# Kernel optimization log

Measured on AMD Instinct MI355X. Metric: run time of the kernel, lower is better.

## Reference

```python
import jax, jax.numpy as jnp
import numpy as np

DT = 1e-4  # integration step, matches Model(dt=0.0001)
T = 4_000_000


def setup_inputs() -> dict:
    key = jax.random.key(0)
    ks = jax.random.split(key, 8)
    inputs = jax.random.normal(ks[0], (1, T, 3), dtype=jnp.float32)
    # time column made increasing (as in a real signal record)
    t = jnp.arange(T, dtype=jnp.float32) * DT
    inputs = inputs.at[0, :, 0].set(t)
    # small-scale 2x2 system matrices; A shifted toward -0.5*I so the
    # 4M-step linear recurrence is stable (no overflow over long horizons)
    A = -0.5 * jnp.eye(2, dtype=jnp.float32) + 0.05 * jax.random.normal(ks[1], (2, 2), jnp.float32)
    B = 0.1 * jax.random.normal(ks[2], (2, 2), jnp.float32)
    D = 0.1 * jax.random.normal(ks[3], (2, 2), jnp.float32)
    E = 0.1 * jax.random.normal(ks[4], (2, 2), jnp.float32)
    cov_in = 0.1 * jax.random.normal(ks[5], (2, 2), jnp.float32)
    training_params = jax.random.normal(ks[6], (1, 2), jnp.float32)
    initial_states = jnp.zeros((1, 5), dtype=jnp.float32)
    return {"inputs": inputs, "A": A, "B": B, "D": D, "E": E,
            "cov_in": cov_in, "training_params": training_params,
            "initial_states": initial_states}


def reference(inputs, A, B, D, E, cov_in, training_params, initial_states):
    # Faithful to GRCell.call: cov = cov_in every step (new_cov is discarded),
    # so XiCov / XiCovC / transition matrix are time-invariant constants.
    dt = jnp.float32(DT)
    sqrt2 = jnp.sqrt(jnp.float32(2.0))
    x_signal = jnp.array([1.0, 0.0], dtype=inputs.dtype)
    XiCov = (E - cov_in @ B) / sqrt2                      # (2,2)
    XiCovC = XiCov @ (-sqrt2 * B.T)                       # (2,2)
    Trans = jnp.eye(2, dtype=inputs.dtype) + (A - XiCovC) * dt  # I + (A-XiCovC)dt
    Cout = -sqrt2 * B.T * dt                              # output map, (2,2)
    p0 = training_params[0, 0]
    p1 = training_params[0, 1]
    seq = inputs[0]                                       # [T, 3] = (time, dy1, dy2)

    def step(x, inp):
        t = inp[0]
        dy = inp[1:]
        out = Cout @ x                                    # emitted BEFORE update
        x_new = Trans @ x + XiCov @ dy + (p0 * jnp.cos(p1 * t) * dt) * x_signal
        return x_new, out

    x0 = initial_states[0, :2]
    _, outs = jax.lax.scan(step, x0, seq)                 # outs: [T, 2]
    return outs[None]                                     # [1, T, 2]
```

## Files before the change

### kernel.cpp

```cpp
#include <hip/hip_runtime.h>
#include <math.h>


constexpr int   TN    = 4000000;
constexpr float FDT   = 1e-4f;
constexpr int   L     = 16;
constexpr int   K     = TN / L;
constexpr int   BT    = 256;
constexpr int   NT    = (K + BT - 1) / BT;
constexpr int   ROWF4 = 9;
constexpr int   F4IN  = TN * 3 / 4;
constexpr int   F4OUT = TN * 2 / 4;

struct Consts {
  float T00, T01, T10, T11;
  float X00, X01, X10, X11;
  float C00, C01, C10, C11;
  float p0, p1;
};

__device__ inline Consts make_consts(const float* __restrict__ A,
                                     const float* __restrict__ B,
                                     const float* __restrict__ E,
                                     const float* __restrict__ cov,
                                     const float* __restrict__ tp) {
  const float s2 = 1.41421356237309515f;
  Consts c;
  float Xi[2][2];
  for (int i = 0; i < 2; ++i)
    for (int j = 0; j < 2; ++j)
      Xi[i][j] = (E[i*2+j] - (cov[i*2+0]*B[0*2+j] + cov[i*2+1]*B[1*2+j])) / s2;
  float XiC[2][2];
  for (int i = 0; i < 2; ++i)
    for (int j = 0; j < 2; ++j)
      XiC[i][j] = Xi[i][0]*(-s2*B[j*2+0]) + Xi[i][1]*(-s2*B[j*2+1]);
  c.T00 = 1.0f + (A[0] - XiC[0][0]) * FDT;
  c.T01 =        (A[1] - XiC[0][1]) * FDT;
  c.T10 =        (A[2] - XiC[1][0]) * FDT;
  c.T11 = 1.0f + (A[3] - XiC[1][1]) * FDT;
  c.X00 = Xi[0][0]; c.X01 = Xi[0][1]; c.X10 = Xi[1][0]; c.X11 = Xi[1][1];
  c.C00 = -s2 * B[0] * FDT;
  c.C01 = -s2 * B[2] * FDT;
  c.C10 = -s2 * B[1] * FDT;
  c.C11 = -s2 * B[3] * FDT;
  c.p0 = tp[0]; c.p1 = tp[1];
  return c;
}

__device__ inline void step(float& x0, float& x1, float t, float a, float b,
                            const Consts& c) {
  float u0 = fmaf(c.X00, a, fmaf(c.X01, b, c.p0 * __cosf(c.p1 * t) * FDT));
  float u1 = fmaf(c.X10, a, c.X11 * b);
  float n0 = fmaf(c.T00, x0, fmaf(c.T01, x1, u0));
  float n1 = fmaf(c.T10, x0, fmaf(c.T11, x1, u1));
  x0 = n0; x1 = n1;
}

__device__ inline void fsq(float* M) {
  float a = M[0]*M[0] + M[1]*M[2];
  float b = M[0]*M[1] + M[1]*M[3];
  float d = M[2]*M[0] + M[3]*M[2];
  float e = M[2]*M[1] + M[3]*M[3];
  M[0] = a; M[1] = b; M[2] = d; M[3] = e;
}

__device__ inline void mulleft(const float* P, float* M) {
  float a0 = P[0]*M[0] + P[1]*M[2];
  float a1 = P[0]*M[1] + P[1]*M[3];
  float a2 = P[2]*M[0] + P[3]*M[2];
  float a3 = P[2]*M[1] + P[3]*M[3];
  M[0]=a0; M[1]=a1; M[2]=a2; M[3]=a3;
}

__device__ inline void powmat8(const float* M, int e, float* R) {
  float C[4] = {M[0], M[1], M[2], M[3]};
  R[0] = 1.f; R[1] = 0.f; R[2] = 0.f; R[3] = 1.f;
  #pragma unroll
  for (int b = 0; b < 8; ++b) {
    if ((e >> b) & 1) mulleft(C, R);
    fsq(C);
  }
}

__global__ void __launch_bounds__(BT, 4)
k1(const float* __restrict__ seq, const float* __restrict__ A,
   const float* __restrict__ B, const float* __restrict__ E,
   const float* __restrict__ cov, const float* __restrict__ tp,
   float2* __restrict__ agg) {
  __shared__ float wg[4][2];
  const int tid  = threadIdx.x;
  const int lane = tid & 63;
  const int w    = tid >> 6;
  const int tile = blockIdx.x;
  Consts c = make_consts(A, B, E, cov, tp);

  const float4* s4 = (const float4*)seq;
  const size_t base = (size_t)tile * 3072 + 3 * tid;
  const float4 z4 = make_float4(0.f, 0.f, 0.f, 0.f);
  float4 v[12];
  #pragma unroll
  for (int it = 0; it < 4; ++it) {
    size_t g = base + (size_t)(it * 768);
    v[3*it+0] = (g     < (size_t)F4IN) ? s4[g]     : z4;
    v[3*it+1] = (g + 1 < (size_t)F4IN) ? s4[g + 1] : z4;
    v[3*it+2] = (g + 2 < (size_t)F4IN) ? s4[g + 2] : z4;
  }

  float S[4] = {c.T00, c.T01, c.T10, c.T11};
  fsq(S); fsq(S);
  float R[4];
  powmat8(S, 255 - tid, R);
  float S256[4] = {S[0], S[1], S[2], S[3]};
  #pragma unroll
  for (int i = 0; i < 8; ++i) fsq(S256);

  float acc0 = 0.f, acc1 = 0.f;
  #pragma unroll
  for (int it = 3; it >= 0; --it) {
    float x0 = 0.f, x1 = 0.f;
    const float4 a = v[3*it], b = v[3*it+1], d = v[3*it+2];
    const int st0 = tile * 4096 + 1024 * it + 4 * tid;
    step(x0, x1, (float)(st0    ) * FDT, a.y, a.z, c);
    step(x0, x1, (float)(st0 + 1) * FDT, b.x, b.y, c);
    step(x0, x1, (float)(st0 + 2) * FDT, b.w, d.x, c);
    step(x0, x1, (float)(st0 + 3) * FDT, d.z, d.w, c);
    if (it != 3) mulleft(S256, R);
    acc0 += R[0]*x0 + R[1]*x1;
    acc1 += R[2]*x0 + R[3]*x1;
  }

  #pragma unroll
  for (int m = 1; m < 64; m <<= 1) {
    acc0 += __shfl_xor(acc0, m);
    acc1 += __shfl_xor(acc1, m);
  }
  if (lane == 0) { wg[w][0] = acc0; wg[w][1] = acc1; }
  __syncthreads();
  if (tid == 0) {
    float a0 = wg[0][0] + wg[1][0] + wg[2][0] + wg[3][0];
    float a1 = wg[0][1] + wg[1][1] + wg[2][1] + wg[3][1];
    agg[tile] = make_float2(a0, a1);
  }
}

__device__ inline void stage_tile(const float4* __restrict__ seq4, int tile,
                                  float4* __restrict__ ls, int tid) {
  const size_t base4 = (size_t)tile * 3072;
  #pragma unroll
  for (int it = 0; it < 4; ++it) {
    const int u = it * BT + tid;
    const size_t g = base4 + (size_t)(it * 768 + 3 * tid);
    float4 v0 = make_float4(0.f,0.f,0.f,0.f);
    float4 v1 = v0, v2 = v0;
    if (g     < (size_t)F4IN) v0 = seq4[g];
    if (g + 1 < (size_t)F4IN) v1 = seq4[g + 1];
    if (g + 2 < (size_t)F4IN) v2 = seq4[g + 2];
    const int st  = u >> 2;
    const int kq  = u & 3;
    const int rot = (st >> 3) & 7;
    float4* row = ls + st * ROWF4;
    row[(2*kq     + rot) & 7] = make_float4(v0.y, v0.z, v1.x, v1.y);
    row[(2*kq + 1 + rot) & 7] = make_float4(v1.w, v2.x, v2.z, v2.w);
  }
}

__global__ void __launch_bounds__(BT, 4)
k3(const float* __restrict__ seq, const float* __restrict__ A,
   const float* __restrict__ B, const float* __restrict__ E,
   const float* __restrict__ cov, const float* __restrict__ tp,
   const float* __restrict__ ini, const float2* __restrict__ agg,
   float* __restrict__ out) {
  __shared__ float4 ls[BT * ROWF4];
  __shared__ float  wg[4][2];
  __shared__ float  sY[2];
  const int tid  = threadIdx.x;
  const int lane = tid & 63;
  const int w    = tid >> 6;
  const int tile = blockIdx.x;
  Consts c = make_consts(A, B, E, cov, tp);

  stage_tile((const float4*)seq, tile, ls, tid);

  {
    float Qb[4] = {c.T00, c.T01, c.T10, c.T11};
    #pragma unroll
    for (int i = 0; i < 12; ++i) fsq(Qb);
    float i0 = 0.f, i1 = 0.f;
    float inc[4][2];
    #pragma unroll
    for (int j = 0; j < 4; ++j) {
      int idx = 4 * tid + j;
      float e0 = 0.f, e1 = 0.f;
      if (idx == 0)      { e0 = ini[0]; e1 = ini[1]; }
      else if (idx < NT) { float2 a = agg[idx-1]; e0 = a.x; e1 = a.y; }
      float n0 = fmaf(Qb[0], i0, fmaf(Qb[1], i1, e0));
      float n1 = fmaf(Qb[2], i0, fmaf(Qb[3], i1, e1));
      i0 = n0; i1 = n1;
      inc[j][0] = i0; inc[j][1] = i1;
    }
    float Q4[4] = {Qb[0], Qb[1], Qb[2], Qb[3]};
    fsq(Q4); fsq(Q4);
    float C[4] = {Q4[0], Q4[1], Q4[2], Q4[3]};
    float v0 = i0, v1 = i1;
    #pragma unroll
    for (int s = 0; s < 6; ++s) {
      int st = 1 << s;
      float p0 = __shfl_up(v0, st);
      float p1 = __shfl_up(v1, st);
      if (lane >= st) {
        float n0 = fmaf(C[0], p0, fmaf(C[1], p1, v0));
        float n1 = fmaf(C[2], p0, fmaf(C[3], p1, v1));
        v0 = n0; v1 = n1;
      }
      fsq(C);
    }
    if (lane == 63) { wg[w][0] = v0; wg[w][1] = v1; }
    __syncthreads();
    float F0 = 0.f, F1 = 0.f;
    for (int ww = 0; ww < w; ++ww) {
      float n0 = fmaf(C[0], F0, fmaf(C[1], F1, wg[ww][0]));
      float n1 = fmaf(C[2], F0, fmaf(C[3], F1, wg[ww][1]));
      F0 = n0; F1 = n1;
    }
    float q0 = __shfl_up(v0, 1);
    float q1 = __shfl_up(v1, 1);
    if (lane == 0) { q0 = 0.f; q1 = 0.f; }
    float Mq[4];
    powmat8(Q4, lane, Mq);
    float Eth0 = fmaf(Mq[0], F0, fmaf(Mq[1], F1, q0));
    float Eth1 = fmaf(Mq[2], F0, fmaf(Mq[3], F1, q1));
    if (tid == (tile >> 2)) {
      int j = tile & 3;
      float Rj[4] = {Qb[0], Qb[1], Qb[2], Qb[3]};
      for (int m = 0; m < j; ++m) mulleft(Qb, Rj);
      sY[0] = fmaf(Rj[0], Eth0, fmaf(Rj[1], Eth1, inc[j][0]));
      sY[1] = fmaf(Rj[2], Eth0, fmaf(Rj[3], Eth1, inc[j][1]));
    }
    __syncthreads();
  }

  float Pb[4] = {c.T00, c.T01, c.T10, c.T11};
  #pragma unroll
  for (int i = 0; i < 4; ++i) fsq(Pb);
  float4* row = &ls[tid * ROWF4];
  const int rot = (tid >> 3) & 7;
  const int gstep = (tile * BT + tid) * L;
  float xe0, xe1;
  {
    float x0 = 0.f, x1 = 0.f;
    #pragma unroll
    for (int q = 0; q < 8; ++q) {
      float4 d = row[(q + rot) & 7];
      step(x0, x1, (float)(gstep + 2*q)     * FDT, d.x, d.y, c);
      step(x0, x1, (float)(gstep + 2*q + 1) * FDT, d.z, d.w, c);
    }
    float C[4] = {Pb[0], Pb[1], Pb[2], Pb[3]};
    float v0 = x0, v1 = x1;
    #pragma unroll
    for (int s = 0; s < 6; ++s) {
      int st = 1 << s;
      float p0 = __shfl_up(v0, st);
      float p1 = __shfl_up(v1, st);
      if (lane >= st) {
        float n0 = fmaf(C[0], p0, fmaf(C[1], p1, v0));
        float n1 = fmaf(C[2], p0, fmaf(C[3], p1, v1));
        v0 = n0; v1 = n1;
      }
      fsq(C);
    }
    if (lane == 63) { wg[w][0] = v0; wg[w][1] = v1; }
    __syncthreads();
    float E0 = 0.f, E1 = 0.f;
    for (int ww = 0; ww < w; ++ww) {
      float n0 = fmaf(C[0], E0, fmaf(C[1], E1, wg[ww][0]));
      float n1 = fmaf(C[2], E0, fmaf(C[3], E1, wg[ww][1]));
      E0 = n0; E1 = n1;
    }
    float pv0 = __shfl_up(v0, 1);
    float pv1 = __shfl_up(v1, 1);
    if (lane == 0) { pv0 = 0.f; pv1 = 0.f; }
    float Ml[4];
    powmat8(Pb, lane, Ml);
    xe0 = fmaf(Ml[0], E0, fmaf(Ml[1], E1, pv0));
    xe1 = fmaf(Ml[2], E0, fmaf(Ml[3], E1, pv1));
  }

  float Mt[4];
  powmat8(Pb, tid, Mt);
  float y0 = sY[0], y1 = sY[1];
  float x0 = fmaf(Mt[0], y0, fmaf(Mt[1], y1, xe0));
  float x1 = fmaf(Mt[2], y0, fmaf(Mt[3], y1, xe1));

  #pragma unroll
  for (int q = 0; q < 8; ++q) {
    float4 d = row[(q + rot) & 7];
    float4 o;
    o.x = fmaf(c.C00, x0, c.C01 * x1); o.y = fmaf(c.C10, x0, c.C11 * x1);
    step(x0, x1, (float)(gstep + 2*q) * FDT, d.x, d.y, c);
    o.z = fmaf(c.C00, x0, c.C01 * x1); o.w = fmaf(c.C10, x0, c.C11 * x1);
    step(x0, x1, (float)(gstep + 2*q + 1) * FDT, d.z, d.w, c);
    row[(q + rot) & 7] = o;
  }
  __syncthreads();

  float4* out4 = (float4*)out;
  const size_t obase = (size_t)tile * 2048;
  #pragma unroll
  for (int i = 0; i < 8; ++i) {
    int lf = i * BT + tid;
    size_t g = obase + (size_t)lf;
    if (g < (size_t)F4OUT) {
      int cc = lf >> 3, s = lf & 7;
      int rc = (cc >> 3) & 7;
      out4[g] = ls[cc * ROWF4 + ((s + rc) & 7)];
    }
  }
}

extern "C" void kernel_launch(void* const* d_in, const int* in_sizes, int n_in,
                              void* d_out, int out_size, void* d_ws, size_t ws_size,
                              hipStream_t stream) {
  const float* seq = (const float*)d_in[0];
  const float* A   = (const float*)d_in[1];
  const float* B   = (const float*)d_in[2];
  const float* E   = (const float*)d_in[4];
  const float* cov = (const float*)d_in[5];
  const float* tp  = (const float*)d_in[6];
  const float* ini = (const float*)d_in[7];
  float* out = (float*)d_out;

  float2* agg = (float2*)d_ws;

  k1<<<NT, BT, 0, stream>>>(seq, A, B, E, cov, tp, agg);
  k3<<<NT, BT, 0, stream>>>(seq, A, B, E, cov, tp, ini, agg, out);
}
```

Baseline: 124.0 us.

## Fuse the two scan passes into one cooperative kernel with a grid-wide sync

The two kernels are merged into one cooperative kernel. Each block stages its input tile in LDS once, computes its local scan and block aggregate, waits at a grid-wide barrier, then resolves the cross-block carry and writes its outputs from the same staged data. This drops the second full read of the input sequence and one kernel launch. In exchange it needs every block resident at once, since the barrier deadlocks otherwise, and it pays for a grid-sync. If the cooperative launch is rejected, it falls back to the old two-kernel path.

```diff
diff --git a/kernel.cpp b/kernel.cpp
--- a/kernel.cpp
+++ b/kernel.cpp
@@ -1,5 +1,8 @@
 #include <hip/hip_runtime.h>
+#include <hip/hip_cooperative_groups.h>
 #include <math.h>
+
+namespace cg = cooperative_groups;
 
 
 constexpr int   TN    = 4000000;
@@ -82,67 +85,6 @@
   }
 }
 
-__global__ void __launch_bounds__(BT, 4)
-k1(const float* __restrict__ seq, const float* __restrict__ A,
-   const float* __restrict__ B, const float* __restrict__ E,
-   const float* __restrict__ cov, const float* __restrict__ tp,
-   float2* __restrict__ agg) {
-  __shared__ float wg[4][2];
-  const int tid  = threadIdx.x;
-  const int lane = tid & 63;
-  const int w    = tid >> 6;
-  const int tile = blockIdx.x;
-  Consts c = make_consts(A, B, E, cov, tp);
-
-  const float4* s4 = (const float4*)seq;
-  const size_t base = (size_t)tile * 3072 + 3 * tid;
-  const float4 z4 = make_float4(0.f, 0.f, 0.f, 0.f);
-  float4 v[12];
-  #pragma unroll
-  for (int it = 0; it < 4; ++it) {
-    size_t g = base + (size_t)(it * 768);
-    v[3*it+0] = (g     < (size_t)F4IN) ? s4[g]     : z4;
-    v[3*it+1] = (g + 1 < (size_t)F4IN) ? s4[g + 1] : z4;
-    v[3*it+2] = (g + 2 < (size_t)F4IN) ? s4[g + 2] : z4;
-  }
-
-  float S[4] = {c.T00, c.T01, c.T10, c.T11};
-  fsq(S); fsq(S);
-  float R[4];
-  powmat8(S, 255 - tid, R);
-  float S256[4] = {S[0], S[1], S[2], S[3]};
-  #pragma unroll
-  for (int i = 0; i < 8; ++i) fsq(S256);
-
-  float acc0 = 0.f, acc1 = 0.f;
-  #pragma unroll
-  for (int it = 3; it >= 0; --it) {
-    float x0 = 0.f, x1 = 0.f;
-    const float4 a = v[3*it], b = v[3*it+1], d = v[3*it+2];
-    const int st0 = tile * 4096 + 1024 * it + 4 * tid;
-    step(x0, x1, (float)(st0    ) * FDT, a.y, a.z, c);
-    step(x0, x1, (float)(st0 + 1) * FDT, b.x, b.y, c);
-    step(x0, x1, (float)(st0 + 2) * FDT, b.w, d.x, c);
-    step(x0, x1, (float)(st0 + 3) * FDT, d.z, d.w, c);
-    if (it != 3) mulleft(S256, R);
-    acc0 += R[0]*x0 + R[1]*x1;
-    acc1 += R[2]*x0 + R[3]*x1;
-  }
-
-  #pragma unroll
-  for (int m = 1; m < 64; m <<= 1) {
-    acc0 += __shfl_xor(acc0, m);
-    acc1 += __shfl_xor(acc1, m);
-  }
-  if (lane == 0) { wg[w][0] = acc0; wg[w][1] = acc1; }
-  __syncthreads();
-  if (tid == 0) {
-    float a0 = wg[0][0] + wg[1][0] + wg[2][0] + wg[3][0];
-    float a1 = wg[0][1] + wg[1][1] + wg[2][1] + wg[3][1];
-    agg[tile] = make_float2(a0, a1);
-  }
-}
-
 __device__ inline void stage_tile(const float4* __restrict__ seq4, int tile,
                                   float4* __restrict__ ls, int tid) {
   const size_t base4 = (size_t)tile * 3072;
@@ -165,6 +107,229 @@
 }
 
 __global__ void __launch_bounds__(BT, 4)
+fused(const float* __restrict__ seq, const float* __restrict__ A,
+      const float* __restrict__ B, const float* __restrict__ E,
+      const float* __restrict__ cov, const float* __restrict__ tp,
+      const float* __restrict__ ini, float2* __restrict__ agg,
+      float* __restrict__ out) {
+  __shared__ float4 ls[BT * ROWF4];
+  __shared__ float  wg[4][2];
+  __shared__ float  sY[2];
+  const int tid  = threadIdx.x;
+  const int lane = tid & 63;
+  const int w    = tid >> 6;
+  const int tile = blockIdx.x;
+  Consts c = make_consts(A, B, E, cov, tp);
+
+  stage_tile((const float4*)seq, tile, ls, tid);
+  __syncthreads();
+
+  float Pb[4] = {c.T00, c.T01, c.T10, c.T11};
+  #pragma unroll
+  for (int i = 0; i < 4; ++i) fsq(Pb);
+  float4* row = &ls[tid * ROWF4];
+  const int rot = (tid >> 3) & 7;
+  const int gstep = (tile * BT + tid) * L;
+
+  float xe0, xe1;
+  {
+    float x0 = 0.f, x1 = 0.f;
+    #pragma unroll
+    for (int q = 0; q < 8; ++q) {
+      float4 d = row[(q + rot) & 7];
+      step(x0, x1, (float)(gstep + 2*q)     * FDT, d.x, d.y, c);
+      step(x0, x1, (float)(gstep + 2*q + 1) * FDT, d.z, d.w, c);
+    }
+    float C[4] = {Pb[0], Pb[1], Pb[2], Pb[3]};
+    float v0 = x0, v1 = x1;
+    #pragma unroll
+    for (int s = 0; s < 6; ++s) {
+      int st = 1 << s;
+      float p0 = __shfl_up(v0, st);
+      float p1 = __shfl_up(v1, st);
+      if (lane >= st) {
+        float n0 = fmaf(C[0], p0, fmaf(C[1], p1, v0));
+        float n1 = fmaf(C[2], p0, fmaf(C[3], p1, v1));
+        v0 = n0; v1 = n1;
+      }
+      fsq(C);
+    }
+    if (lane == 63) { wg[w][0] = v0; wg[w][1] = v1; }
+    __syncthreads();
+    float E0 = 0.f, E1 = 0.f;
+    for (int ww = 0; ww < w; ++ww) {
+      float n0 = fmaf(C[0], E0, fmaf(C[1], E1, wg[ww][0]));
+      float n1 = fmaf(C[2], E0, fmaf(C[3], E1, wg[ww][1]));
+      E0 = n0; E1 = n1;
+    }
+    float pv0 = __shfl_up(v0, 1);
+    float pv1 = __shfl_up(v1, 1);
+    if (lane == 0) { pv0 = 0.f; pv1 = 0.f; }
+    float Ml[4];
+    powmat8(Pb, lane, Ml);
+    xe0 = fmaf(Ml[0], E0, fmaf(Ml[1], E1, pv0));
+    xe1 = fmaf(Ml[2], E0, fmaf(Ml[3], E1, pv1));
+    if (tid == BT - 1) {
+      float a0 = fmaf(C[0], E0, fmaf(C[1], E1, v0));
+      float a1 = fmaf(C[2], E0, fmaf(C[3], E1, v1));
+      agg[tile] = make_float2(a0, a1);
+    }
+  }
+
+  cg::this_grid().sync();
+
+  {
+    float Qb[4] = {c.T00, c.T01, c.T10, c.T11};
+    #pragma unroll
+    for (int i = 0; i < 12; ++i) fsq(Qb);
+    float i0 = 0.f, i1 = 0.f;
+    float inc[4][2];
+    #pragma unroll
+    for (int j = 0; j < 4; ++j) {
+      int idx = 4 * tid + j;
+      float e0 = 0.f, e1 = 0.f;
+      if (idx == 0)      { e0 = ini[0]; e1 = ini[1]; }
+      else if (idx < NT) { float2 a = agg[idx-1]; e0 = a.x; e1 = a.y; }
+      float n0 = fmaf(Qb[0], i0, fmaf(Qb[1], i1, e0));
+      float n1 = fmaf(Qb[2], i0, fmaf(Qb[3], i1, e1));
+      i0 = n0; i1 = n1;
+      inc[j][0] = i0; inc[j][1] = i1;
+    }
+    float Q4[4] = {Qb[0], Qb[1], Qb[2], Qb[3]};
+    fsq(Q4); fsq(Q4);
+    float C[4] = {Q4[0], Q4[1], Q4[2], Q4[3]};
+    float v0 = i0, v1 = i1;
+    #pragma unroll
+    for (int s = 0; s < 6; ++s) {
+      int st = 1 << s;
+      float p0 = __shfl_up(v0, st);
+      float p1 = __shfl_up(v1, st);
+      if (lane >= st) {
+        float n0 = fmaf(C[0], p0, fmaf(C[1], p1, v0));
+        float n1 = fmaf(C[2], p0, fmaf(C[3], p1, v1));
+        v0 = n0; v1 = n1;
+      }
+      fsq(C);
+    }
+    if (lane == 63) { wg[w][0] = v0; wg[w][1] = v1; }
+    __syncthreads();
+    float F0 = 0.f, F1 = 0.f;
+    for (int ww = 0; ww < w; ++ww) {
+      float n0 = fmaf(C[0], F0, fmaf(C[1], F1, wg[ww][0]));
+      float n1 = fmaf(C[2], F0, fmaf(C[3], F1, wg[ww][1]));
+      F0 = n0; F1 = n1;
+    }
+    float q0 = __shfl_up(v0, 1);
+    float q1 = __shfl_up(v1, 1);
+    if (lane == 0) { q0 = 0.f; q1 = 0.f; }
+    float Mq[4];
+    powmat8(Q4, lane, Mq);
+    float Eth0 = fmaf(Mq[0], F0, fmaf(Mq[1], F1, q0));
+    float Eth1 = fmaf(Mq[2], F0, fmaf(Mq[3], F1, q1));
+    if (tid == (tile >> 2)) {
+      int j = tile & 3;
+      float Rj[4] = {Qb[0], Qb[1], Qb[2], Qb[3]};
+      for (int m = 0; m < j; ++m) mulleft(Qb, Rj);
+      sY[0] = fmaf(Rj[0], Eth0, fmaf(Rj[1], Eth1, inc[j][0]));
+      sY[1] = fmaf(Rj[2], Eth0, fmaf(Rj[3], Eth1, inc[j][1]));
+    }
+    __syncthreads();
+  }
+
+  float Mt[4];
+  powmat8(Pb, tid, Mt);
+  float y0 = sY[0], y1 = sY[1];
+  float x0 = fmaf(Mt[0], y0, fmaf(Mt[1], y1, xe0));
+  float x1 = fmaf(Mt[2], y0, fmaf(Mt[3], y1, xe1));
+
+  #pragma unroll
+  for (int q = 0; q < 8; ++q) {
+    float4 d = row[(q + rot) & 7];
+    float4 o;
+    o.x = fmaf(c.C00, x0, c.C01 * x1); o.y = fmaf(c.C10, x0, c.C11 * x1);
+    step(x0, x1, (float)(gstep + 2*q) * FDT, d.x, d.y, c);
+    o.z = fmaf(c.C00, x0, c.C01 * x1); o.w = fmaf(c.C10, x0, c.C11 * x1);
+    step(x0, x1, (float)(gstep + 2*q + 1) * FDT, d.z, d.w, c);
+    row[(q + rot) & 7] = o;
+  }
+  __syncthreads();
+
+  float4* out4 = (float4*)out;
+  const size_t obase = (size_t)tile * 2048;
+  #pragma unroll
+  for (int i = 0; i < 8; ++i) {
+    int lf = i * BT + tid;
+    size_t g = obase + (size_t)lf;
+    if (g < (size_t)F4OUT) {
+      int cc = lf >> 3, s = lf & 7;
+      int rc = (cc >> 3) & 7;
+      out4[g] = ls[cc * ROWF4 + ((s + rc) & 7)];
+    }
+  }
+}
+
+__global__ void __launch_bounds__(BT, 4)
+k1(const float* __restrict__ seq, const float* __restrict__ A,
+   const float* __restrict__ B, const float* __restrict__ E,
+   const float* __restrict__ cov, const float* __restrict__ tp,
+   float2* __restrict__ agg) {
+  __shared__ float wg[4][2];
+  const int tid  = threadIdx.x;
+  const int lane = tid & 63;
+  const int w    = tid >> 6;
+  const int tile = blockIdx.x;
+  Consts c = make_consts(A, B, E, cov, tp);
+
+  const float4* s4 = (const float4*)seq;
+  const size_t base = (size_t)tile * 3072 + 3 * tid;
+  const float4 z4 = make_float4(0.f, 0.f, 0.f, 0.f);
+  float4 v[12];
+  #pragma unroll
+  for (int it = 0; it < 4; ++it) {
+    size_t g = base + (size_t)(it * 768);
+    v[3*it+0] = (g     < (size_t)F4IN) ? s4[g]     : z4;
+    v[3*it+1] = (g + 1 < (size_t)F4IN) ? s4[g + 1] : z4;
+    v[3*it+2] = (g + 2 < (size_t)F4IN) ? s4[g + 2] : z4;
+  }
+
+  float S[4] = {c.T00, c.T01, c.T10, c.T11};
+  fsq(S); fsq(S);
+  float R[4];
+  powmat8(S, 255 - tid, R);
+  float S256[4] = {S[0], S[1], S[2], S[3]};
+  #pragma unroll
+  for (int i = 0; i < 8; ++i) fsq(S256);
+
+  float acc0 = 0.f, acc1 = 0.f;
+  #pragma unroll
+  for (int it = 3; it >= 0; --it) {
+    float x0 = 0.f, x1 = 0.f;
+    const float4 a = v[3*it], b = v[3*it+1], d = v[3*it+2];
+    const int st0 = tile * 4096 + 1024 * it + 4 * tid;
+    step(x0, x1, (float)(st0    ) * FDT, a.y, a.z, c);
+    step(x0, x1, (float)(st0 + 1) * FDT, b.x, b.y, c);
+    step(x0, x1, (float)(st0 + 2) * FDT, b.w, d.x, c);
+    step(x0, x1, (float)(st0 + 3) * FDT, d.z, d.w, c);
+    if (it != 3) mulleft(S256, R);
+    acc0 += R[0]*x0 + R[1]*x1;
+    acc1 += R[2]*x0 + R[3]*x1;
+  }
+
+  #pragma unroll
+  for (int m = 1; m < 64; m <<= 1) {
+    acc0 += __shfl_xor(acc0, m);
+    acc1 += __shfl_xor(acc1, m);
+  }
+  if (lane == 0) { wg[w][0] = acc0; wg[w][1] = acc1; }
+  __syncthreads();
+  if (tid == 0) {
+    float a0 = wg[0][0] + wg[1][0] + wg[2][0] + wg[3][0];
+    float a1 = wg[0][1] + wg[1][1] + wg[2][1] + wg[3][1];
+    agg[tile] = make_float2(a0, a1);
+  }
+}
+
+__global__ void __launch_bounds__(BT, 4)
 k3(const float* __restrict__ seq, const float* __restrict__ A,
    const float* __restrict__ B, const float* __restrict__ E,
    const float* __restrict__ cov, const float* __restrict__ tp,
@@ -331,6 +496,12 @@
 
   float2* agg = (float2*)d_ws;
 
-  k1<<<NT, BT, 0, stream>>>(seq, A, B, E, cov, tp, agg);
-  k3<<<NT, BT, 0, stream>>>(seq, A, B, E, cov, tp, ini, agg, out);
-}
+  void* args[] = {(void*)&seq, (void*)&A, (void*)&B, (void*)&E, (void*)&cov,
+                  (void*)&tp, (void*)&ini, (void*)&agg, (void*)&out};
+  hipError_t err = hipLaunchCooperativeKernel((void*)fused, dim3(NT), dim3(BT),
+                                              args, 0, stream);
+  if (err != hipSuccess) {
+    k1<<<NT, BT, 0, stream>>>(seq, A, B, E, cov, tp, agg);
+    k3<<<NT, BT, 0, stream>>>(seq, A, B, E, cov, tp, ini, agg, out);
+  }
+}
```

After: 272.7 us. +119.9%, slower.

## Fuse two-pass scan into single-pass decoupled look-back kernel

Applied to the files above, without the earlier changes.

Replaces the separate aggregate kernel and the scan-of-aggregates prologue with one kernel. Each block publishes its local aggregate and inclusive prefix through flagged 64-bit atomics, and wave 0 spins with a windowed look-back over up to 64 predecessors. The goal is to read the input once instead of twice and to drop one kernel launch. In exchange it adds a memset of the flag workspace, depends on blocks being scheduled in order to make progress, and serialises tiles through the inter-block spin wait.

```diff
diff --git a/kernel.cpp b/kernel.cpp
--- a/kernel.cpp
+++ b/kernel.cpp
@@ -1,6 +1,8 @@
 #include <hip/hip_runtime.h>
 #include <math.h>
 
+
+typedef unsigned long long ull;
 
 constexpr int   TN    = 4000000;
 constexpr float FDT   = 1e-4f;
@@ -11,6 +13,7 @@
 constexpr int   ROWF4 = 9;
 constexpr int   F4IN  = TN * 3 / 4;
 constexpr int   F4OUT = TN * 2 / 4;
+constexpr ull   SENT  = ~0ull;
 
 struct Consts {
   float T00, T01, T10, T11;
@@ -82,65 +85,16 @@
   }
 }
 
-__global__ void __launch_bounds__(BT, 4)
-k1(const float* __restrict__ seq, const float* __restrict__ A,
-   const float* __restrict__ B, const float* __restrict__ E,
-   const float* __restrict__ cov, const float* __restrict__ tp,
-   float2* __restrict__ agg) {
-  __shared__ float wg[4][2];
-  const int tid  = threadIdx.x;
-  const int lane = tid & 63;
-  const int w    = tid >> 6;
-  const int tile = blockIdx.x;
-  Consts c = make_consts(A, B, E, cov, tp);
-
-  const float4* s4 = (const float4*)seq;
-  const size_t base = (size_t)tile * 3072 + 3 * tid;
-  const float4 z4 = make_float4(0.f, 0.f, 0.f, 0.f);
-  float4 v[12];
-  #pragma unroll
-  for (int it = 0; it < 4; ++it) {
-    size_t g = base + (size_t)(it * 768);
-    v[3*it+0] = (g     < (size_t)F4IN) ? s4[g]     : z4;
-    v[3*it+1] = (g + 1 < (size_t)F4IN) ? s4[g + 1] : z4;
-    v[3*it+2] = (g + 2 < (size_t)F4IN) ? s4[g + 2] : z4;
-  }
-
-  float S[4] = {c.T00, c.T01, c.T10, c.T11};
-  fsq(S); fsq(S);
-  float R[4];
-  powmat8(S, 255 - tid, R);
-  float S256[4] = {S[0], S[1], S[2], S[3]};
-  #pragma unroll
-  for (int i = 0; i < 8; ++i) fsq(S256);
-
-  float acc0 = 0.f, acc1 = 0.f;
-  #pragma unroll
-  for (int it = 3; it >= 0; --it) {
-    float x0 = 0.f, x1 = 0.f;
-    const float4 a = v[3*it], b = v[3*it+1], d = v[3*it+2];
-    const int st0 = tile * 4096 + 1024 * it + 4 * tid;
-    step(x0, x1, (float)(st0    ) * FDT, a.y, a.z, c);
-    step(x0, x1, (float)(st0 + 1) * FDT, b.x, b.y, c);
-    step(x0, x1, (float)(st0 + 2) * FDT, b.w, d.x, c);
-    step(x0, x1, (float)(st0 + 3) * FDT, d.z, d.w, c);
-    if (it != 3) mulleft(S256, R);
-    acc0 += R[0]*x0 + R[1]*x1;
-    acc1 += R[2]*x0 + R[3]*x1;
-  }
-
-  #pragma unroll
-  for (int m = 1; m < 64; m <<= 1) {
-    acc0 += __shfl_xor(acc0, m);
-    acc1 += __shfl_xor(acc1, m);
-  }
-  if (lane == 0) { wg[w][0] = acc0; wg[w][1] = acc1; }
-  __syncthreads();
-  if (tid == 0) {
-    float a0 = wg[0][0] + wg[1][0] + wg[2][0] + wg[3][0];
-    float a1 = wg[0][1] + wg[1][1] + wg[2][1] + wg[3][1];
-    agg[tile] = make_float2(a0, a1);
-  }
+__device__ inline ull pack2(float a, float b) {
+  float2 t = make_float2(a, b);
+  ull r;
+  __builtin_memcpy(&r, &t, 8);
+  return r;
+}
+__device__ inline float2 unpack2(ull v) {
+  float2 t;
+  __builtin_memcpy(&t, &v, 8);
+  return t;
 }
 
 __device__ inline void stage_tile(const float4* __restrict__ seq4, int tile,
@@ -165,13 +119,14 @@
 }
 
 __global__ void __launch_bounds__(BT, 4)
-k3(const float* __restrict__ seq, const float* __restrict__ A,
-   const float* __restrict__ B, const float* __restrict__ E,
-   const float* __restrict__ cov, const float* __restrict__ tp,
-   const float* __restrict__ ini, const float2* __restrict__ agg,
-   float* __restrict__ out) {
+fused(const float* __restrict__ seq, const float* __restrict__ A,
+      const float* __restrict__ B, const float* __restrict__ E,
+      const float* __restrict__ cov, const float* __restrict__ tp,
+      const float* __restrict__ ini, ull* __restrict__ aggP,
+      ull* __restrict__ inclP, float* __restrict__ out) {
   __shared__ float4 ls[BT * ROWF4];
   __shared__ float  wg[4][2];
+  __shared__ float  sA[2];
   __shared__ float  sY[2];
   const int tid  = threadIdx.x;
   const int lane = tid & 63;
@@ -180,64 +135,7 @@
   Consts c = make_consts(A, B, E, cov, tp);
 
   stage_tile((const float4*)seq, tile, ls, tid);
-
-  {
-    float Qb[4] = {c.T00, c.T01, c.T10, c.T11};
-    #pragma unroll
-    for (int i = 0; i < 12; ++i) fsq(Qb);
-    float i0 = 0.f, i1 = 0.f;
-    float inc[4][2];
-    #pragma unroll
-    for (int j = 0; j < 4; ++j) {
-      int idx = 4 * tid + j;
-      float e0 = 0.f, e1 = 0.f;
-      if (idx == 0)      { e0 = ini[0]; e1 = ini[1]; }
-      else if (idx < NT) { float2 a = agg[idx-1]; e0 = a.x; e1 = a.y; }
-      float n0 = fmaf(Qb[0], i0, fmaf(Qb[1], i1, e0));
-      float n1 = fmaf(Qb[2], i0, fmaf(Qb[3], i1, e1));
-      i0 = n0; i1 = n1;
-      inc[j][0] = i0; inc[j][1] = i1;
-    }
-    float Q4[4] = {Qb[0], Qb[1], Qb[2], Qb[3]};
-    fsq(Q4); fsq(Q4);
-    float C[4] = {Q4[0], Q4[1], Q4[2], Q4[3]};
-    float v0 = i0, v1 = i1;
-    #pragma unroll
-    for (int s = 0; s < 6; ++s) {
-      int st = 1 << s;
-      float p0 = __shfl_up(v0, st);
-      float p1 = __shfl_up(v1, st);
-      if (lane >= st) {
-        float n0 = fmaf(C[0], p0, fmaf(C[1], p1, v0));
-        float n1 = fmaf(C[2], p0, fmaf(C[3], p1, v1));
-        v0 = n0; v1 = n1;
-      }
-      fsq(C);
-    }
-    if (lane == 63) { wg[w][0] = v0; wg[w][1] = v1; }
-    __syncthreads();
-    float F0 = 0.f, F1 = 0.f;
-    for (int ww = 0; ww < w; ++ww) {
-      float n0 = fmaf(C[0], F0, fmaf(C[1], F1, wg[ww][0]));
-      float n1 = fmaf(C[2], F0, fmaf(C[3], F1, wg[ww][1]));
-      F0 = n0; F1 = n1;
-    }
-    float q0 = __shfl_up(v0, 1);
-    float q1 = __shfl_up(v1, 1);
-    if (lane == 0) { q0 = 0.f; q1 = 0.f; }
-    float Mq[4];
-    powmat8(Q4, lane, Mq);
-    float Eth0 = fmaf(Mq[0], F0, fmaf(Mq[1], F1, q0));
-    float Eth1 = fmaf(Mq[2], F0, fmaf(Mq[3], F1, q1));
-    if (tid == (tile >> 2)) {
-      int j = tile & 3;
-      float Rj[4] = {Qb[0], Qb[1], Qb[2], Qb[3]};
-      for (int m = 0; m < j; ++m) mulleft(Qb, Rj);
-      sY[0] = fmaf(Rj[0], Eth0, fmaf(Rj[1], Eth1, inc[j][0]));
-      sY[1] = fmaf(Rj[2], Eth0, fmaf(Rj[3], Eth1, inc[j][1]));
-    }
-    __syncthreads();
-  }
+  __syncthreads();
 
   float Pb[4] = {c.T00, c.T01, c.T10, c.T11};
   #pragma unroll
@@ -245,6 +143,7 @@
   float4* row = &ls[tid * ROWF4];
   const int rot = (tid >> 3) & 7;
   const int gstep = (tile * BT + tid) * L;
+
   float xe0, xe1;
   {
     float x0 = 0.f, x1 = 0.f;
@@ -283,7 +182,80 @@
     powmat8(Pb, lane, Ml);
     xe0 = fmaf(Ml[0], E0, fmaf(Ml[1], E1, pv0));
     xe1 = fmaf(Ml[2], E0, fmaf(Ml[3], E1, pv1));
-  }
+    if (tid == BT - 1) {
+      sA[0] = fmaf(C[0], E0, fmaf(C[1], E1, v0));
+      sA[1] = fmaf(C[2], E0, fmaf(C[3], E1, v1));
+    }
+  }
+  __syncthreads();
+
+  float Qb[4] = {c.T00, c.T01, c.T10, c.T11};
+  #pragma unroll
+  for (int i = 0; i < 12; ++i) fsq(Qb);
+  if (w == 0) {
+    if (lane == 0)
+      __hip_atomic_store(&aggP[tile], pack2(sA[0], sA[1]),
+                         __ATOMIC_RELEASE, __HIP_MEMORY_SCOPE_AGENT);
+    float y0, y1;
+    if (tile == 0) {
+      y0 = ini[0]; y1 = ini[1];
+    } else {
+      float Ql[4];
+      powmat8(Qb, lane, Ql);
+      const int j = tile - 1 - lane;
+      const bool hasj = (j >= 0);
+      bool ird = false, ard = !hasj;
+      ull ival = SENT, aval = 0;
+      int lstar;
+      while (true) {
+        if (hasj && !ird) {
+          ival = __hip_atomic_load(&inclP[j], __ATOMIC_ACQUIRE,
+                                   __HIP_MEMORY_SCOPE_AGENT);
+          ird = (ival != SENT);
+        }
+        if (hasj && !ard) {
+          aval = __hip_atomic_load(&aggP[j], __ATOMIC_ACQUIRE,
+                                   __HIP_MEMORY_SCOPE_AGENT);
+          ard = (aval != SENT);
+        }
+        ull im = __ballot(ird);
+        ull am = __ballot(ard || ird);
+        if (im) {
+          int ls_ = __ffsll(im) - 1;
+          ull need = (ls_ == 0) ? 0ull : ((1ull << ls_) - 1ull);
+          if ((am & need) == need) { lstar = ls_; break; }
+        }
+        __builtin_amdgcn_s_sleep(4);
+      }
+      float c0 = 0.f, c1 = 0.f;
+      if (lane < lstar) {
+        if (!ard)
+          aval = __hip_atomic_load(&aggP[j], __ATOMIC_ACQUIRE,
+                                   __HIP_MEMORY_SCOPE_AGENT);
+        float2 g = unpack2(aval);
+        c0 = Ql[0]*g.x + Ql[1]*g.y;
+        c1 = Ql[2]*g.x + Ql[3]*g.y;
+      } else if (lane == lstar) {
+        float2 g = unpack2(ival);
+        c0 = Ql[0]*g.x + Ql[1]*g.y;
+        c1 = Ql[2]*g.x + Ql[3]*g.y;
+      }
+      #pragma unroll
+      for (int m = 1; m < 64; m <<= 1) {
+        c0 += __shfl_xor(c0, m);
+        c1 += __shfl_xor(c1, m);
+      }
+      y0 = c0; y1 = c1;
+    }
+    if (lane == 0) {
+      sY[0] = y0; sY[1] = y1;
+      float i0 = fmaf(Qb[0], y0, fmaf(Qb[1], y1, sA[0]));
+      float i1 = fmaf(Qb[2], y0, fmaf(Qb[3], y1, sA[1]));
+      __hip_atomic_store(&inclP[tile], pack2(i0, i1),
+                         __ATOMIC_RELEASE, __HIP_MEMORY_SCOPE_AGENT);
+    }
+  }
+  __syncthreads();
 
   float Mt[4];
   powmat8(Pb, tid, Mt);
@@ -329,8 +301,9 @@
   const float* ini = (const float*)d_in[7];
   float* out = (float*)d_out;
 
-  float2* agg = (float2*)d_ws;
-
-  k1<<<NT, BT, 0, stream>>>(seq, A, B, E, cov, tp, agg);
-  k3<<<NT, BT, 0, stream>>>(seq, A, B, E, cov, tp, ini, agg, out);
-}
+  ull* aggP  = (ull*)d_ws;
+  ull* inclP = (ull*)((char*)d_ws + 8192);
+
+  hipMemsetAsync(d_ws, 0xFF, 16384, stream);
+  fused<<<NT, BT, 0, stream>>>(seq, A, B, E, cov, tp, ini, aggP, inclP, out);
+}
```

New measurement: 275.1 us. 122% more time.
